# Optimization experiments

Hardware: AMD Instinct MI355X
Metric: run time of the kernel (lower is better)

## Reference

```python
import math
import jax, jax.numpy as jnp
import numpy as np

HEADS, HD = 16, 64  # head_dim = hidden_size // num_heads = 1024 // 16

def _c(a):
    # a: [2, ...] stacked (real, imag) -> complex64
    return jax.lax.complex(a[0], a[1])

def setup_inputs() -> dict:
    key = jax.random.key(0)
    ks = jax.random.split(key, 16)
    B, S, L, H = 2, 2048, 2048, 1024  # batch, chunk len, cache len, hidden
    w_scale = 1.0 / math.sqrt(2 * H)  # complex fan-in scaling
    d = {
        "hidden":  jax.random.normal(ks[0], (2, B, S, H), jnp.float32),
        "k_cache": jax.random.normal(ks[1], (2, B, L, HEADS, HD), jnp.float32),
        "v_cache": jax.random.normal(ks[2], (2, B, L, HEADS, HD), jnp.float32),
        "qw": jax.random.normal(ks[3], (2, H, H), jnp.float32) * w_scale,
        "qb": jax.random.normal(ks[4], (2, H), jnp.float32) * 0.01,
        "kw": jax.random.normal(ks[5], (2, H, H), jnp.float32) * w_scale,
        "kb": jax.random.normal(ks[6], (2, H), jnp.float32) * 0.01,
        "vw": jax.random.normal(ks[7], (2, H, H), jnp.float32) * w_scale,
        "vb": jax.random.normal(ks[8], (2, H), jnp.float32) * 0.01,
        "ow": jax.random.normal(ks[9], (2, H, H), jnp.float32) * w_scale,
        "ob": jax.random.normal(ks[10], (2, H), jnp.float32) * 0.01,
        "ln_gamma": jnp.stack([jnp.ones(H, jnp.float32) + 0.01 * jax.random.normal(ks[11], (H,)),
                               0.01 * jax.random.normal(ks[12], (H,))]),
        "ln_beta":  0.01 * jax.random.normal(ks[13], (2, H), jnp.float32),
    }
    return d

def _complex_layernorm(x, gamma, beta, eps=1e-5):
    mu = jnp.mean(x, axis=-1, keepdims=True)              # complex mean
    xc = x - mu
    var = jnp.mean(xc.real**2 + xc.imag**2, axis=-1, keepdims=True)
    return xc / jnp.sqrt(var + eps) * gamma + beta

def _clin(z, w, b):
    # complex linear: z [..., in] @ W^T [out, in] + b [out]
    return jnp.einsum('bsh,oh->bso', z, _c(w)) + _c(b)

def reference(hidden, k_cache, v_cache, qw, qb, kw, kb, vw, vb, ow, ob, ln_gamma, ln_beta):
    x = _c(hidden)                                        # [B,S,H] complex64
    B, S, H = x.shape
    normed = _complex_layernorm(x, _c(ln_gamma), _c(ln_beta))
    Q = _clin(normed, qw, qb).reshape(B, S, HEADS, HD)
    K_new = _clin(normed, kw, kb).reshape(B, S, HEADS, HD)
    V_new = _clin(normed, vw, vb).reshape(B, S, HEADS, HD)
    K = jnp.concatenate([_c(k_cache), K_new], axis=1)     # [B, L+S, nh, hd]
    V = jnp.concatenate([_c(v_cache), V_new], axis=1)
    cache_len = k_cache.shape[2]
    kv = K.shape[1]                                       # == window_size here
    # Hermitian score: Re(Q K^dagger) / sqrt(hd)
    scores = jnp.einsum('bqhd,bkhd->bhqk', Q, jnp.conj(K)).real / math.sqrt(HD)
    row = jnp.arange(S)[:, None]
    col = jnp.arange(kv)[None, :]
    # prefix (cache) fully visible; causal within the new chunk
    mask = jnp.where((col >= cache_len) & (col - cache_len > row), -jnp.inf, 0.0).astype(scores.dtype)
    w = jax.nn.softmax(scores + mask[None, None], axis=-1)  # real weights
    out = jax.lax.complex(jnp.einsum('bhqk,bkhd->bqhd', w, V.real),
                          jnp.einsum('bhqk,bkhd->bqhd', w, V.imag)).reshape(B, S, H)
    delta = _clin(out, ow, ob)
    y = x + delta
    out_stacked = jnp.stack([y.real, y.imag])             # [2,B,S,H]
    new_k = jnp.stack([K.real, K.imag])                   # [2,B,window,nh,hd]
    new_v = jnp.stack([V.real, V.imag])
    return (out_stacked, new_k, new_v)
```

## Files before the change

### kernel.cpp

```cpp
#include <hip/hip_runtime.h>

#define HEADS 16
#define SEQ   2048
#define HID   1024
#define CACHE 2048
#define KVLEN 4096
#define MROWS 4096
#define KD    2048

typedef float  f32x4  __attribute__((ext_vector_type(4)));
typedef __bf16 bf16x4 __attribute__((ext_vector_type(4)));
typedef __bf16 bf16x8 __attribute__((ext_vector_type(8)));

__device__ __forceinline__ void gload_lds16(const void* g, void* l) {
  __builtin_amdgcn_global_load_lds((const __attribute__((address_space(1))) void*)g,
                                   (__attribute__((address_space(3))) void*)l, 16, 0, 0);
}

__global__ __launch_bounds__(256) void k_layernorm(const float* __restrict__ hid,
                                                   const float* __restrict__ gamma,
                                                   const float* __restrict__ beta,
                                                   __bf16* __restrict__ normed) {
  int row = blockIdx.x;
  int t = threadIdx.x;
  const float* xr = hid + (size_t)row * HID;
  const float* xi = hid + (size_t)MROWS * HID + (size_t)row * HID;
  float vr[4], vi[4];
  float sr = 0.f, si = 0.f;
#pragma unroll
  for (int i = 0; i < 4; i++) { int h = t + i * 256; vr[i] = xr[h]; vi[i] = xi[h]; sr += vr[i]; si += vi[i]; }
  __shared__ float red[2][4];
  for (int m = 1; m < 64; m <<= 1) { sr += __shfl_xor(sr, m); si += __shfl_xor(si, m); }
  int wid = t >> 6, l = t & 63;
  if (l == 0) { red[0][wid] = sr; red[1][wid] = si; }
  __syncthreads();
  float mr = (red[0][0] + red[0][1] + red[0][2] + red[0][3]) * (1.0f / HID);
  float mi = (red[1][0] + red[1][1] + red[1][2] + red[1][3]) * (1.0f / HID);
  float sv = 0.f;
#pragma unroll
  for (int i = 0; i < 4; i++) { float a = vr[i] - mr, b = vi[i] - mi; sv += a * a + b * b; }
  for (int m = 1; m < 64; m <<= 1) sv += __shfl_xor(sv, m);
  __syncthreads();
  if (l == 0) red[0][wid] = sv;
  __syncthreads();
  float var = (red[0][0] + red[0][1] + red[0][2] + red[0][3]) * (1.0f / HID);
  float inv = rsqrtf(var + 1e-5f);
  __bf16* outr = normed + (size_t)row * KD;
#pragma unroll
  for (int i = 0; i < 4; i++) {
    int h = t + i * 256;
    float a = (vr[i] - mr) * inv, b = (vi[i] - mi) * inv;
    float gr = gamma[h], gi = gamma[HID + h], br = beta[h], bi = beta[HID + h];
    outr[h]       = (__bf16)(a * gr - b * gi + br);
    outr[HID + h] = (__bf16)(a * gi + b * gr + bi);
  }
}

__global__ __launch_bounds__(256) void k_packw(const float* __restrict__ qw, const float* __restrict__ kw,
                                               const float* __restrict__ vw, const float* __restrict__ ow,
                                               __bf16* __restrict__ dst) {
  int idx = blockIdx.x * 256 + threadIdx.x;
  int sel = idx >> 19;
  int li  = idx & 524287;
  const float* w = sel == 0 ? qw : (sel == 1 ? kw : (sel == 2 ? vw : ow));
  int o  = li >> 8;
  int k0 = (li & 255) * 8;
  const float* wr = w;
  const float* wi = w + HID * HID;
  int oimag = (o >= HID);
  int oo = o & (HID - 1);
  bf16x8 v;
#pragma unroll
  for (int j = 0; j < 8; j++) {
    int k = k0 + j;
    int kim = (k >= HID);
    int kk = k & (HID - 1);
    float x;
    if (!oimag) x = kim ? -wi[oo * HID + kk] : wr[oo * HID + kk];
    else        x = kim ?  wr[oo * HID + kk] : wi[oo * HID + kk];
    v[j] = (__bf16)x;
  }
  *(bf16x8*)(dst + ((size_t)sel << 22) + (size_t)o * KD + k0) = v;
}

__global__ __launch_bounds__(256) void k_copykv(const float* __restrict__ kc, const float* __restrict__ vc,
                                                float* __restrict__ nk, float* __restrict__ nv,
                                                __bf16* __restrict__ Ka) {
  int i = blockIdx.x * 256 + threadIdx.x;
  int sel = i >> 21;
  int li = i & ((1 << 21) - 1);
  if (sel == 0) {
    int c4 = li & 255;
    int kv = (li >> 8) & 2047;
    int b  = (li >> 19) & 1;
    int p  = (li >> 20) & 1;
    f32x4 v = *(const f32x4*)(kc + (((size_t)((p * 2 + b) * 2048 + kv)) << 10) + c4 * 4);
    *(f32x4*)(nk + ((((size_t)(p * 2 + b)) * KVLEN + kv) << 10) + c4 * 4) = v;
    int h = c4 >> 4, d = (c4 & 15) * 4;
    bf16x4 w;
#pragma unroll
    for (int j = 0; j < 4; j++) w[j] = (__bf16)v[j];
    *(bf16x4*)(Ka + (((size_t)(b * 16 + h)) * KVLEN + kv) * 128 + p * 64 + d) = w;
  } else {
    size_t sf = (size_t)li << 2;
    size_t chunk = sf >> 21;
    size_t df = sf + (chunk << 21);
    *(f32x4*)(nv + df) = *(const f32x4*)(vc + sf);
  }
}

__global__ __launch_bounds__(256) void k_buildv(const float* __restrict__ vc, __bf16* __restrict__ dst) {
  __shared__ float tile[32][129];
  int kt = blockIdx.x;
  int bh = blockIdx.y;
  int b = bh >> 4, h = bh & 15;
  int t = threadIdx.x;
  int kv0 = kt * 32;
#pragma unroll
  for (int i = 0; i < 16; i++) {
    int idx = i * 256 + t;
    int kvl = idx >> 7, dsl = idx & 127;
    int p = dsl >> 6, d = dsl & 63;
    tile[kvl][dsl] = vc[(((size_t)(p * 2 + b)) * CACHE + kv0 + kvl) * HID + h * 64 + d];
  }
  __syncthreads();
#pragma unroll
  for (int i = 0; i < 16; i++) {
    int idx = i * 256 + t;
    int dsl = idx >> 5, kvl = idx & 31;
    dst[(((size_t)bh) * 128 + dsl) * KVLEN + kv0 + kvl] = (__bf16)tile[kvl][dsl];
  }
}

#define BM 128
#define BN 128
#define BK 64
template <int QKV>
__global__ __launch_bounds__(256, 3) void k_gemm(const __bf16* __restrict__ A,
                                                 const __bf16* __restrict__ Bp,
                                                 const float* __restrict__ bias0,
                                                 const float* __restrict__ bias1,
                                                 const float* __restrict__ bias2,
                                                 const float* __restrict__ hid,
                                                 float* __restrict__ outF0,
                                                 float* __restrict__ outF1,
                                                 __bf16* __restrict__ outB0,
                                                 __bf16* __restrict__ outB1,
                                                 __bf16* __restrict__ outB2) {
  __shared__ __align__(16) __bf16 As[BM * BK];
  __shared__ __align__(16) __bf16 Bs[BN * BK];
  int bm0 = blockIdx.x * BM, bn0 = blockIdx.y * BN;
  int t = threadIdx.x, l = t & 63, wid = t >> 6;
  int wr = wid >> 1, wc = wid & 1;
  int l15 = l & 15, lg = l >> 4;
  f32x4 acc[4][4];
  f32x4 zero = {0.f, 0.f, 0.f, 0.f};
#pragma unroll
  for (int i = 0; i < 4; i++)
#pragma unroll
    for (int j = 0; j < 4; j++) acc[i][j] = zero;
  const __bf16* Ab = A + (size_t)bm0 * KD;
  const __bf16* Bb = Bp + (size_t)bn0 * KD;
  for (int k0 = 0; k0 < KD; k0 += BK) {
#pragma unroll
    for (int c = 0; c < 4; c++) {
      int idx = c * 256 + t;
      int row = idx >> 3, ch = idx & 7;
      gload_lds16(Ab + (size_t)row * KD + k0 + ch * 8, As + idx * 8);
      gload_lds16(Bb + (size_t)row * KD + k0 + ch * 8, Bs + idx * 8);
    }
    __syncthreads();
#pragma unroll
    for (int ks = 0; ks < 2; ks++) {
      bf16x8 af[4], bfv[4];
#pragma unroll
      for (int i = 0; i < 4; i++) {
        af[i]  = *(const bf16x8*)(As + (wr * 64 + i * 16 + l15) * BK + ks * 32 + lg * 8);
        bfv[i] = *(const bf16x8*)(Bs + (wc * 64 + i * 16 + l15) * BK + ks * 32 + lg * 8);
      }
#pragma unroll
      for (int mi = 0; mi < 4; mi++)
#pragma unroll
        for (int ni = 0; ni < 4; ni++)
          acc[mi][ni] = __builtin_amdgcn_mfma_f32_16x16x32_bf16(af[mi], bfv[ni], acc[mi][ni], 0, 0, 0);
    }
    __syncthreads();
  }
#pragma unroll
  for (int mi = 0; mi < 4; mi++) {
#pragma unroll
    for (int ni = 0; ni < 4; ni++) {
      int mbase = bm0 + wr * 64 + mi * 16 + lg * 4;
      int n = bn0 + wc * 64 + ni * 16 + l15;
      int b = mbase >> 11, sbase = mbase & 2047;
      if (QKV) {
        int mode = n >> 11, nl = n & 2047;
        const float* bias = mode == 0 ? bias0 : (mode == 1 ? bias1 : bias2);
        float bv = bias[nl];
        int p = nl >> 10, hd = nl & 1023;
        if (mode == 2) {
          bf16x4 w;
#pragma unroll
          for (int j = 0; j < 4; j++) {
            float v = acc[mi][ni][j] + bv;
            outF1[(((size_t)(p * 2 + b)) * KVLEN + (CACHE + sbase + j)) * HID + hd] = v;
            w[j] = (__bf16)v;
          }
          *(bf16x4*)(outB2 + (((size_t)(b * 16 + (hd >> 6))) * 128 + p * 64 + (hd & 63)) * KVLEN + CACHE + sbase) = w;
        } else {
#pragma unroll
          for (int j = 0; j < 4; j++) {
            float v = acc[mi][ni][j] + bv;
            int s = sbase + j;
            if (mode == 0) {
              outB0[(((size_t)(b * 16 + (hd >> 6))) * SEQ + s) * 128 + p * 64 + (hd & 63)] = (__bf16)v;
            } else {
              outF0[(((size_t)(p * 2 + b)) * KVLEN + (CACHE + s)) * HID + hd] = v;
              outB1[(((size_t)(b * 16 + (hd >> 6))) * KVLEN + (CACHE + s)) * 128 + p * 64 + (hd & 63)] = (__bf16)v;
            }
          }
        }
      } else {
        float bv = bias0[n];
        int p = n >> 10;
#pragma unroll
        for (int j = 0; j < 4; j++) {
          float v = acc[mi][ni][j] + bv;
          size_t off = (((size_t)(p * 2 + b)) * SEQ + (sbase + j)) * HID + (n & 1023);
          outF0[off] = v + hid[off];
        }
      }
    }
  }
}

__global__ __launch_bounds__(256, 2) void k_attn(const __bf16* __restrict__ Q,
                                                 const __bf16* __restrict__ Kt,
                                                 const __bf16* __restrict__ Vt,
                                                 __bf16* __restrict__ outp) {
  __shared__ __align__(16) __bf16 Ks[2][64 * 128];
  __shared__ __align__(16) __bf16 Vs[2][128 * 64];
  __shared__ __align__(16) __bf16 Ps[4][32 * 64];
  int id = blockIdx.y * gridDim.x + blockIdx.x;
  int xcd = id & 7, li = id >> 3;
  int bh = (xcd << 2) | (li >> 4);
  int ql = li & 15;
  int qt = (ql & 1) ? (15 - (ql >> 1)) : (ql >> 1);
  int b = bh >> 4, h = bh & 15;
  int t = threadIdx.x, l = t & 63, wid = t >> 6;
  int l15 = l & 15, lg = l >> 4;
  const __bf16* Qb = Q + ((size_t)bh * SEQ) * 128;
  const __bf16* Kb = Kt + ((size_t)bh * KVLEN) * 128;
  const __bf16* Vb = Vt + ((size_t)bh * 128) * KVLEN;
  __bf16* Pw = &Ps[wid][0];
  int q0 = qt * 128 + wid * 32;
  bf16x8 aQ[2][4];
#pragma unroll
  for (int mi = 0; mi < 2; mi++)
#pragma unroll
    for (int dk = 0; dk < 4; dk++)
      aQ[mi][dk] = *(const bf16x8*)(Qb + (size_t)(q0 + mi * 16 + l15) * 128 + dk * 32 + lg * 8);
  f32x4 zero = {0.f, 0.f, 0.f, 0.f};
  f32x4 o[2][8];
  f32x4 sums[2];
#pragma unroll
  for (int mi = 0; mi < 2; mi++) {
    sums[mi] = zero;
#pragma unroll
    for (int df = 0; df < 8; df++) o[mi][df] = zero;
  }
  bf16x8 ones;
#pragma unroll
  for (int i = 0; i < 8; i++) ones[i] = (__bf16)1.0f;
  const int nfull = 32 + 2 * qt;
  const int nt = nfull + 2;
  int sw = (l15 & 7) << 4;

  auto STAGE = [&](int bb, int ti) {
    int kv0 = ti * 64;
#pragma unroll
    for (int c = 0; c < 4; c++) {
      int idx = c * 256 + t;
      int kr = idx >> 4;
      gload_lds16(Kb + (size_t)(kv0 + kr) * 128 + (((idx & 15) ^ (kr & 7)) << 3), &Ks[bb][idx * 8]);
      int vr = idx >> 3;
      gload_lds16(Vb + (size_t)vr * KVLEN + kv0 + (((idx & 7) ^ (vr & 7)) << 3), &Vs[bb][idx * 8]);
    }
  };

  STAGE(0, 0);
  for (int ti = 0; ti < nt; ti++) {
    int bb = ti & 1;
    if (ti + 1 < nt) {
      STAGE(bb ^ 1, ti + 1);
      asm volatile("s_waitcnt vmcnt(8)" ::: "memory");
    } else {
      asm volatile("s_waitcnt vmcnt(0)" ::: "memory");
    }
    __builtin_amdgcn_s_barrier();
    const char* KsB = (const char*)&Ks[bb][0];
    const char* VsB = (const char*)&Vs[bb][0];
    f32x4 sacc[2][4];
    __builtin_amdgcn_s_setprio(1);
#pragma unroll
    for (int kvf = 0; kvf < 4; kvf++) {
      sacc[0][kvf] = zero; sacc[1][kvf] = zero;
      const char* kbase = KsB + (kvf * 16 + l15) * 256;
#pragma unroll
      for (int dk = 0; dk < 4; dk++) {
        bf16x8 bK = *(const bf16x8*)(kbase + ((dk * 64 + lg * 16) ^ sw));
        sacc[0][kvf] = __builtin_amdgcn_mfma_f32_16x16x32_bf16(bK, aQ[0][dk], sacc[0][kvf], 0, 0, 0);
        sacc[1][kvf] = __builtin_amdgcn_mfma_f32_16x16x32_bf16(bK, aQ[1][dk], sacc[1][kvf], 0, 0, 0);
      }
    }
    __builtin_amdgcn_s_setprio(0);
    bool masked = (ti >= nfull);
#pragma unroll
    for (int mi = 0; mi < 2; mi++) {
      int row = mi * 16 + l15;
      int rx = (row & 7) << 3;
#pragma unroll
      for (int kvf = 0; kvf < 4; kvf++) {
        bf16x4 w;
#pragma unroll
        for (int j = 0; j < 4; j++) {
          float p = exp2f(sacc[mi][kvf][j] * 0.18033688011112042f);
          if (masked) {
            int cg = ti * 64 + kvf * 16 + lg * 4 + j - CACHE;
            if (cg > q0 + row - qt * 128 + qt * 128) p = p;
            if (cg > qt * 128 + wid * 32 + row) p = 0.f;
          }
          w[j] = (__bf16)p;
        }
        *(bf16x4*)(Pw + row * 64 + ((kvf * 16 + lg * 4) ^ rx)) = w;
      }
    }
    bf16x8 bV[2][8], aP[2][2];
#pragma unroll
    for (int ks = 0; ks < 2; ks++) {
      int off = (ks * 64 + lg * 16) ^ sw;
#pragma unroll
      for (int df = 0; df < 8; df++)
        bV[ks][df] = *(const bf16x8*)(VsB + (df * 16 + l15) * 128 + off);
    }
#pragma unroll
    for (int mi = 0; mi < 2; mi++) {
      int row = mi * 16 + l15;
      int rx = (row & 7) << 3;
      const __bf16* pb = Pw + row * 64;
#pragma unroll
      for (int ks = 0; ks < 2; ks++)
        aP[mi][ks] = *(const bf16x8*)(pb + ((ks * 32 + lg * 8) ^ rx));
    }
    __builtin_amdgcn_s_setprio(1);
#pragma unroll
    for (int mi = 0; mi < 2; mi++) {
#pragma unroll
      for (int ks = 0; ks < 2; ks++) {
        sums[mi] = __builtin_amdgcn_mfma_f32_16x16x32_bf16(aP[mi][ks], ones, sums[mi], 0, 0, 0);
#pragma unroll
        for (int df = 0; df < 8; df++)
          o[mi][df] = __builtin_amdgcn_mfma_f32_16x16x32_bf16(aP[mi][ks], bV[ks][df], o[mi][df], 0, 0, 0);
      }
    }
    __builtin_amdgcn_s_setprio(0);
    __builtin_amdgcn_s_barrier();
  }
#pragma unroll
  for (int mi = 0; mi < 2; mi++) {
    float inv[4];
#pragma unroll
    for (int j = 0; j < 4; j++) inv[j] = 1.0f / sums[mi][j];
#pragma unroll
    for (int df = 0; df < 8; df++) {
      int dslot = df * 16 + l15;
      int col = (dslot < 64) ? (h * 64 + dslot) : (1024 + h * 64 + (dslot - 64));
#pragma unroll
      for (int j = 0; j < 4; j++) {
        int qg2 = q0 + mi * 16 + lg * 4 + j;
        float v = o[mi][df][j] * inv[j];
        outp[((size_t)(b * SEQ + qg2)) * KD + col] = (__bf16)v;
      }
    }
  }
}

extern "C" void kernel_launch(void* const* d_in, const int* in_sizes, int n_in,
                              void* d_out, int out_size, void* d_ws, size_t ws_size,
                              hipStream_t stream) {
  const float* hid = (const float*)d_in[0];
  const float* kc  = (const float*)d_in[1];
  const float* vc  = (const float*)d_in[2];
  const float* qw  = (const float*)d_in[3];
  const float* qb  = (const float*)d_in[4];
  const float* kw  = (const float*)d_in[5];
  const float* kb  = (const float*)d_in[6];
  const float* vw  = (const float*)d_in[7];
  const float* vb  = (const float*)d_in[8];
  const float* ow  = (const float*)d_in[9];
  const float* ob  = (const float*)d_in[10];
  const float* lg  = (const float*)d_in[11];
  const float* lb  = (const float*)d_in[12];

  float* y  = (float*)d_out;
  float* nk = y + 8388608;
  float* nv = nk + 16777216;

  char* ws = (char*)d_ws;
  __bf16* normed = (__bf16*)(ws);
  __bf16* wall   = (__bf16*)(ws + 16777216);
  __bf16* Qa     = (__bf16*)(ws + 50331648);
  __bf16* Ka     = (__bf16*)(ws + 67108864);
  __bf16* Va     = (__bf16*)(ws + 100663296);
  __bf16* ao     = (__bf16*)(ws + 134217728);

  k_layernorm<<<4096, 256, 0, stream>>>(hid, lg, lb, normed);
  k_packw<<<8192, 256, 0, stream>>>(qw, kw, vw, ow, wall);
  k_copykv<<<16384, 256, 0, stream>>>(kc, vc, nk, nv, Ka);
  dim3 gv(64, 32);
  k_buildv<<<gv, 256, 0, stream>>>(vc, Va);
  dim3 gq(32, 48);
  k_gemm<1><<<gq, 256, 0, stream>>>(normed, wall, qb, kb, vb, nullptr, nk, nv, Qa, Ka, Va);
  dim3 ga(16, 32);
  k_attn<<<ga, 256, 0, stream>>>(Qa, Ka, Va, ao);
  dim3 go(32, 16);
  k_gemm<0><<<go, 256, 0, stream>>>(ao, wall + ((size_t)3 << 22), ob, nullptr, nullptr, hid, y, nullptr, nullptr, nullptr, nullptr);
}
```

Measured before the change: 448.9 us.

## Fuse V cache copy into transpose and register-stage attention K/V tiles

The V-cache copy into the output moves into the V transpose kernel, so the cache is read once instead of twice. The attention kernel drops double-buffered direct-to-LDS loads and prefetches the next K/V tile into registers, writing it to a single LDS buffer after compute. The smaller LDS footprint lets occupancy rise from 2 to 3 blocks per CU. In exchange it adds an extra barrier per tile, more register pressure and less overlap between loads and compute.

```diff
diff --git a/kernel.cpp b/kernel.cpp
--- a/kernel.cpp
+++ b/kernel.cpp
@@ -83,33 +83,26 @@
   *(bf16x8*)(dst + ((size_t)sel << 22) + (size_t)o * KD + k0) = v;
 }
 
-__global__ __launch_bounds__(256) void k_copykv(const float* __restrict__ kc, const float* __restrict__ vc,
-                                                float* __restrict__ nk, float* __restrict__ nv,
-                                                __bf16* __restrict__ Ka) {
-  int i = blockIdx.x * 256 + threadIdx.x;
-  int sel = i >> 21;
-  int li = i & ((1 << 21) - 1);
-  if (sel == 0) {
-    int c4 = li & 255;
-    int kv = (li >> 8) & 2047;
-    int b  = (li >> 19) & 1;
-    int p  = (li >> 20) & 1;
-    f32x4 v = *(const f32x4*)(kc + (((size_t)((p * 2 + b) * 2048 + kv)) << 10) + c4 * 4);
-    *(f32x4*)(nk + ((((size_t)(p * 2 + b)) * KVLEN + kv) << 10) + c4 * 4) = v;
-    int h = c4 >> 4, d = (c4 & 15) * 4;
-    bf16x4 w;
-#pragma unroll
-    for (int j = 0; j < 4; j++) w[j] = (__bf16)v[j];
-    *(bf16x4*)(Ka + (((size_t)(b * 16 + h)) * KVLEN + kv) * 128 + p * 64 + d) = w;
-  } else {
-    size_t sf = (size_t)li << 2;
-    size_t chunk = sf >> 21;
-    size_t df = sf + (chunk << 21);
-    *(f32x4*)(nv + df) = *(const f32x4*)(vc + sf);
-  }
-}
-
-__global__ __launch_bounds__(256) void k_buildv(const float* __restrict__ vc, __bf16* __restrict__ dst) {
+__global__ __launch_bounds__(256) void k_copyk(const float* __restrict__ kc,
+                                               float* __restrict__ nk,
+                                               __bf16* __restrict__ Ka) {
+  int li = blockIdx.x * 256 + threadIdx.x;
+  int c4 = li & 255;
+  int kv = (li >> 8) & 2047;
+  int b  = (li >> 19) & 1;
+  int p  = (li >> 20) & 1;
+  f32x4 v = *(const f32x4*)(kc + (((size_t)((p * 2 + b) * 2048 + kv)) << 10) + c4 * 4);
+  *(f32x4*)(nk + ((((size_t)(p * 2 + b)) * KVLEN + kv) << 10) + c4 * 4) = v;
+  int h = c4 >> 4, d = (c4 & 15) * 4;
+  bf16x4 w;
+#pragma unroll
+  for (int j = 0; j < 4; j++) w[j] = (__bf16)v[j];
+  *(bf16x4*)(Ka + (((size_t)(b * 16 + h)) * KVLEN + kv) * 128 + p * 64 + d) = w;
+}
+
+__global__ __launch_bounds__(256) void k_buildv(const float* __restrict__ vc,
+                                                float* __restrict__ nv,
+                                                __bf16* __restrict__ dst) {
   __shared__ float tile[32][129];
   int kt = blockIdx.x;
   int bh = blockIdx.y;
@@ -121,7 +114,9 @@
     int idx = i * 256 + t;
     int kvl = idx >> 7, dsl = idx & 127;
     int p = dsl >> 6, d = dsl & 63;
-    tile[kvl][dsl] = vc[(((size_t)(p * 2 + b)) * CACHE + kv0 + kvl) * HID + h * 64 + d];
+    float v = vc[(((size_t)(p * 2 + b)) * CACHE + kv0 + kvl) * HID + h * 64 + d];
+    tile[kvl][dsl] = v;
+    nv[(((size_t)(p * 2 + b)) * KVLEN + kv0 + kvl) * HID + h * 64 + d] = v;
   }
   __syncthreads();
 #pragma unroll
@@ -234,12 +229,12 @@
   }
 }
 
-__global__ __launch_bounds__(256, 2) void k_attn(const __bf16* __restrict__ Q,
+__global__ __launch_bounds__(256, 3) void k_attn(const __bf16* __restrict__ Q,
                                                  const __bf16* __restrict__ Kt,
                                                  const __bf16* __restrict__ Vt,
                                                  __bf16* __restrict__ outp) {
-  __shared__ __align__(16) __bf16 Ks[2][64 * 128];
-  __shared__ __align__(16) __bf16 Vs[2][128 * 64];
+  __shared__ __align__(16) __bf16 Ks[64 * 128];
+  __shared__ __align__(16) __bf16 Vs[128 * 64];
   __shared__ __align__(16) __bf16 Ps[4][32 * 64];
   int id = blockIdx.y * gridDim.x + blockIdx.x;
   int xcd = id & 7, li = id >> 3;
@@ -276,30 +271,37 @@
   const int nt = nfull + 2;
   int sw = (l15 & 7) << 4;
 
-  auto STAGE = [&](int bb, int ti) {
+  bf16x8 kreg[4], vreg[4];
+  auto LOADT = [&](int ti) {
     int kv0 = ti * 64;
 #pragma unroll
     for (int c = 0; c < 4; c++) {
       int idx = c * 256 + t;
       int kr = idx >> 4;
-      gload_lds16(Kb + (size_t)(kv0 + kr) * 128 + (((idx & 15) ^ (kr & 7)) << 3), &Ks[bb][idx * 8]);
+      kreg[c] = *(const bf16x8*)(Kb + (size_t)(kv0 + kr) * 128 + (((idx & 15) ^ (kr & 7)) << 3));
       int vr = idx >> 3;
-      gload_lds16(Vb + (size_t)vr * KVLEN + kv0 + (((idx & 7) ^ (vr & 7)) << 3), &Vs[bb][idx * 8]);
+      vreg[c] = *(const bf16x8*)(Vb + (size_t)vr * KVLEN + kv0 + (((idx & 7) ^ (vr & 7)) << 3));
     }
   };
-
-  STAGE(0, 0);
+  auto WRITET = [&]() {
+#pragma unroll
+    for (int c = 0; c < 4; c++) {
+      int idx = c * 256 + t;
+      *(bf16x8*)((char*)Ks + idx * 16) = kreg[c];
+      *(bf16x8*)((char*)Vs + idx * 16) = vreg[c];
+    }
+  };
+
+  LOADT(0);
+  WRITET();
+  __syncthreads();
   for (int ti = 0; ti < nt; ti++) {
-    int bb = ti & 1;
     if (ti + 1 < nt) {
-      STAGE(bb ^ 1, ti + 1);
-      asm volatile("s_waitcnt vmcnt(8)" ::: "memory");
-    } else {
-      asm volatile("s_waitcnt vmcnt(0)" ::: "memory");
-    }
-    __builtin_amdgcn_s_barrier();
-    const char* KsB = (const char*)&Ks[bb][0];
-    const char* VsB = (const char*)&Vs[bb][0];
+      LOADT(ti + 1);
+      __builtin_amdgcn_sched_barrier(0);
+    }
+    const char* KsB = (const char*)&Ks[0];
+    const char* VsB = (const char*)&Vs[0];
     f32x4 sacc[2][4];
     __builtin_amdgcn_s_setprio(1);
 #pragma unroll
@@ -327,7 +329,6 @@
           float p = exp2f(sacc[mi][kvf][j] * 0.18033688011112042f);
           if (masked) {
             int cg = ti * 64 + kvf * 16 + lg * 4 + j - CACHE;
-            if (cg > q0 + row - qt * 128 + qt * 128) p = p;
             if (cg > qt * 128 + wid * 32 + row) p = 0.f;
           }
           w[j] = (__bf16)p;
@@ -364,7 +365,11 @@
       }
     }
     __builtin_amdgcn_s_setprio(0);
-    __builtin_amdgcn_s_barrier();
+    __syncthreads();
+    if (ti + 1 < nt) {
+      WRITET();
+      __syncthreads();
+    }
   }
 #pragma unroll
   for (int mi = 0; mi < 2; mi++) {
@@ -416,9 +421,9 @@
 
   k_layernorm<<<4096, 256, 0, stream>>>(hid, lg, lb, normed);
   k_packw<<<8192, 256, 0, stream>>>(qw, kw, vw, ow, wall);
-  k_copykv<<<16384, 256, 0, stream>>>(kc, vc, nk, nv, Ka);
+  k_copyk<<<8192, 256, 0, stream>>>(kc, nk, Ka);
   dim3 gv(64, 32);
-  k_buildv<<<gv, 256, 0, stream>>>(vc, Va);
+  k_buildv<<<gv, 256, 0, stream>>>(vc, nv, Va);
   dim3 gq(32, 48);
   k_gemm<1><<<gq, 256, 0, stream>>>(normed, wall, qb, kb, vb, nullptr, nk, nv, Qa, Ka, Va);
   dim3 ga(16, 32);
```

New measurement: 1.379 ms. 207% more time.
